# Optimization experiments

Hardware: AMD Instinct MI355X
Metric: run time of the kernel (lower is better)

Reference implementation:

```python
import jax, jax.numpy as jnp
import numpy as np

HEADS = 4
DIM_HEAD = 32
SCALE = DIM_HEAD ** -0.5
EPS = 1e-5


def setup_inputs() -> dict:
    key = jax.random.key(0)
    k1, k2, k3, k4 = jax.random.split(key, 4)
    dim = 256
    hidden = HEADS * DIM_HEAD  # 128
    x = jax.random.normal(k1, (16, dim, 64, 64), dtype=jnp.float32)
    # 1x1 conv weights stored as [out_ch, in_ch] (kernel size 1 squeezed)
    w_qkv = jax.random.normal(k2, (hidden * 3, dim), dtype=jnp.float32) * (dim ** -0.5)
    w_out = jax.random.normal(k3, (dim, hidden), dtype=jnp.float32) * (hidden ** -0.5)
    b_out = jax.random.normal(k4, (dim,), dtype=jnp.float32) * 0.01
    g = jnp.ones((1, dim, 1, 1), dtype=jnp.float32)  # LayerNorm gain
    return {"x": x, "w_qkv": w_qkv, "w_out": w_out, "b_out": b_out, "g": g}


def reference(x, w_qkv, w_out, b_out, g):
    b, c, h, w = x.shape
    n = h * w
    # 1x1 conv to qkv: [b, 3*hidden, h, w]
    qkv = jnp.einsum('oc,bchw->bohw', w_qkv, x)
    q, k, v = jnp.split(qkv, 3, axis=1)

    def to_heads(t):
        return t.reshape(b, HEADS, DIM_HEAD, n)  # b h d n

    q, k, v = to_heads(q), to_heads(k), to_heads(v)
    q = jax.nn.softmax(q, axis=2) * SCALE       # softmax over head-dim d
    k = jax.nn.softmax(k, axis=3)               # softmax over spatial n
    v = v / n                                    # v / (h*w)
    context = jnp.einsum('bhdn,bhen->bhde', k, v)
    out = jnp.einsum('bhde,bhdn->bhen', context, q)  # b h e n
    out = out.reshape(b, HEADS * DIM_HEAD, h, w)
    # output 1x1 conv with bias
    out = jnp.einsum('oc,bchw->bohw', w_out, out) + b_out[None, :, None, None]
    # channel LayerNorm (biased variance over dim=1)
    mean = jnp.mean(out, axis=1, keepdims=True)
    var = jnp.var(out, axis=1, keepdims=True)
    return (out - mean) * jax.lax.rsqrt(var + EPS) * g
```

## Files before the change

kernel.cpp:

```cpp
#include <hip/hip_runtime.h>

typedef short short8 __attribute__((ext_vector_type(8)));
typedef float f32x16 __attribute__((ext_vector_type(16)));
typedef unsigned short ushort_t;

#define B_    16
#define C_    256
#define N_    4096
#define H_    4
#define HID_  128
#define SCALE_ 0.17677669529663687f
#define EPS_  1e-5f

__device__ inline unsigned cvtpk(float a, float b) {
  unsigned r;
  asm("v_cvt_pk_bf16_f32 %0, %1, %2" : "=v"(r) : "v"(a), "v"(b));
  return r;
}

__device__ inline int2 pack4(float a, float b, float c, float d) {
  int2 o;
  o.x = (int)cvtpk(a, b);
  o.y = (int)cvtpk(c, d);
  return o;
}

__device__ inline short8 ld_frag16(const ushort_t* p) {
  return __builtin_bit_cast(short8, *(const int4*)p);
}
__device__ inline short8 ld_frag8(const ushort_t* p) {
  int2 a = *(const int2*)p, b = *(const int2*)(p + 4);
  int4 t; t.x = a.x; t.y = a.y; t.z = b.x; t.w = b.y;
  return __builtin_bit_cast(short8, t);
}

__global__ void k0_wswz(const float* __restrict__ w, ushort_t* __restrict__ wsw) {
  int gid = blockIdx.x * 256 + threadIdx.x;
  int ln = gid & 63, kc = (gid >> 6) & 15, mt = gid >> 10;
  int row = mt * 32 + (ln & 31);
  int col = kc * 16 + (ln >> 5) * 8;
  const float* src = w + (size_t)row * 256 + col;
  float4 a = *(const float4*)src, b = *(const float4*)(src + 4);
  int4 o;
  o.x = (int)cvtpk(a.x, a.y); o.y = (int)cvtpk(a.z, a.w);
  o.z = (int)cvtpk(b.x, b.y); o.w = (int)cvtpk(b.z, b.w);
  *(int4*)(wsw + (size_t)gid * 8) = o;
}

__global__ __launch_bounds__(256, 3) void k1_qkv(
    const float* __restrict__ x, const ushort_t* __restrict__ wsw,
    ushort_t* __restrict__ qp, float* __restrict__ pctx, float* __restrict__ psum)
{
  __shared__ __align__(16) union {
    ushort_t Xs[64 * 264];
    struct { ushort_t kt[128 * 68]; ushort_t vt[128 * 68]; } s2;
  } sm;

  const int tid = threadIdx.x;
  const int b = blockIdx.y;
  const int blk = blockIdx.x;
  const int n0 = blk * 64;
  const int hw = tid >> 6, lane = tid & 63;
  const int half = lane >> 5, lm = lane & 31;

  {
    const float* xsrc = x + (size_t)b * C_ * N_ + n0;
    const int n4 = tid & 15;
    const int cq0 = tid >> 4;
    #pragma unroll
    for (int cc = 0; cc < 4; ++cc) {
      const int cq = cq0 + cc * 16;
      const float* p = xsrc + (size_t)(cq * 4) * N_ + n4 * 4;
      float4 a0 = *(const float4*)(p);
      float4 a1 = *(const float4*)(p + N_);
      float4 a2 = *(const float4*)(p + 2 * N_);
      float4 a3 = *(const float4*)(p + 3 * N_);
      ushort_t* d = sm.Xs + (((cq >> 1) ^ n4) * 8 + (cq & 1) * 4) + (n4 * 4) * 264;
      *(int2*)(d + 0 * 264) = pack4(a0.x, a1.x, a2.x, a3.x);
      *(int2*)(d + 1 * 264) = pack4(a0.y, a1.y, a2.y, a3.y);
      *(int2*)(d + 2 * 264) = pack4(a0.z, a1.z, a2.z, a3.z);
      *(int2*)(d + 3 * 264) = pack4(a0.w, a1.w, a2.w, a3.w);
    }
  }
  __syncthreads();

  f32x16 acc0a, acc0b, acc1a, acc1b, acc2a, acc2b;
  for (int r = 0; r < 16; ++r) {
    acc0a[r] = 0.0f; acc0b[r] = 0.0f; acc1a[r] = 0.0f;
    acc1b[r] = 0.0f; acc2a[r] = 0.0f; acc2b[r] = 0.0f;
  }
  {
    const ushort_t* xrow0 = sm.Xs + lm * 264;
    const ushort_t* xrow1 = sm.Xs + (32 + lm) * 264;
    const int sn0 = lm >> 2;
    const int sn1 = 8 + (lm >> 2);
    const ushort_t* wl = wsw + (size_t)(hw * 16 * 64 + lane) * 8;
    #pragma unroll
    for (int kc = 0; kc < 16; ++kc) {
      short8 b0 = ld_frag16(xrow0 + (((2 * kc + half) ^ sn0) << 3));
      short8 b1 = ld_frag16(xrow1 + (((2 * kc + half) ^ sn1) << 3));
      short8 af0 = ld_frag16(wl + kc * 512);
      short8 af1 = ld_frag16(wl + 32768 + kc * 512);
      short8 af2 = ld_frag16(wl + 65536 + kc * 512);
      acc0a = __builtin_amdgcn_mfma_f32_32x32x16_bf16(af0, b0, acc0a, 0, 0, 0);
      acc0b = __builtin_amdgcn_mfma_f32_32x32x16_bf16(af0, b1, acc0b, 0, 0, 0);
      acc1a = __builtin_amdgcn_mfma_f32_32x32x16_bf16(af1, b0, acc1a, 0, 0, 0);
      acc1b = __builtin_amdgcn_mfma_f32_32x32x16_bf16(af1, b1, acc1b, 0, 0, 0);
      acc2a = __builtin_amdgcn_mfma_f32_32x32x16_bf16(af2, b0, acc2a, 0, 0, 0);
      acc2b = __builtin_amdgcn_mfma_f32_32x32x16_bf16(af2, b1, acc2b, 0, 0, 0);
    }
  }

  __syncthreads();

  for (int r = 0; r < 16; ++r) {
    int row = (r & 3) + 8 * (r >> 2) + 4 * half;
    ushort_t* krow = sm.s2.kt + (hw * 32 + row) * 68;
    ushort_t* vrow = sm.s2.vt + (hw * 32 + row) * 68;
    unsigned kk = cvtpk(__expf(acc1a[r]), __expf(acc1b[r]));
    unsigned vv = cvtpk(acc2a[r], acc2b[r]);
    krow[lm]      = (ushort_t)kk;
    krow[32 + lm] = (ushort_t)(kk >> 16);
    vrow[lm]      = (ushort_t)vv;
    vrow[32 + lm] = (ushort_t)(vv >> 16);
  }
  __syncthreads();

  {
    f32x16 cacc, sacc;
    for (int r = 0; r < 16; ++r) { cacc[r] = 0.0f; sacc[r] = 0.0f; }
    short8 ones;
    #pragma unroll
    for (int j = 0; j < 8; ++j) ones[j] = (short)0x3F80;
    const ushort_t* ka = sm.s2.kt + (hw * 32 + lm) * 68 + half * 8;
    const ushort_t* va = sm.s2.vt + (hw * 32 + lm) * 68 + half * 8;
    #pragma unroll
    for (int ks = 0; ks < 4; ++ks) {
      short8 af = ld_frag8(ka + ks * 16);
      short8 bf = ld_frag8(va + ks * 16);
      cacc = __builtin_amdgcn_mfma_f32_32x32x16_bf16(af, bf, cacc, 0, 0, 0);
      sacc = __builtin_amdgcn_mfma_f32_32x32x16_bf16(af, ones, sacc, 0, 0, 0);
    }

    {
      ushort_t* qpb = qp + (size_t)b * N_ * 128;
      {
        float m = -1e30f;
        for (int r = 0; r < 16; ++r) m = fmaxf(m, acc0a[r]);
        m = fmaxf(m, __shfl_xor(m, 32));
        float qe[16]; float s = 0.0f;
        for (int r = 0; r < 16; ++r) { qe[r] = __expf(acc0a[r] - m); s += qe[r]; }
        s += __shfl_xor(s, 32);
        float sc = SCALE_ / s;
        const int gnt = blk * 2;
        for (int q = 0; q < 4; ++q) {
          int kc = hw * 2 + (q >> 1);
          int fl = (q & 1) * 32 + lm;
          int2 o = pack4(qe[q * 4 + 0] * sc, qe[q * 4 + 1] * sc,
                         qe[q * 4 + 2] * sc, qe[q * 4 + 3] * sc);
          *(int2*)(qpb + (size_t)((gnt * 8 + kc) * 64 + fl) * 8 + 4 * half) = o;
        }
      }
      {
        float m = -1e30f;
        for (int r = 0; r < 16; ++r) m = fmaxf(m, acc0b[r]);
        m = fmaxf(m, __shfl_xor(m, 32));
        float qe[16]; float s = 0.0f;
        for (int r = 0; r < 16; ++r) { qe[r] = __expf(acc0b[r] - m); s += qe[r]; }
        s += __shfl_xor(s, 32);
        float sc = SCALE_ / s;
        const int gnt = blk * 2 + 1;
        for (int q = 0; q < 4; ++q) {
          int kc = hw * 2 + (q >> 1);
          int fl = (q & 1) * 32 + lm;
          int2 o = pack4(qe[q * 4 + 0] * sc, qe[q * 4 + 1] * sc,
                         qe[q * 4 + 2] * sc, qe[q * 4 + 3] * sc);
          *(int2*)(qpb + (size_t)((gnt * 8 + kc) * 64 + fl) * 8 + 4 * half) = o;
        }
      }
    }

    float* pc = pctx + ((size_t)(b * 4 + hw) * 64 + blk) * 1024;
    for (int r = 0; r < 16; ++r) {
      int row = (r & 3) + 8 * (r >> 2) + 4 * half;
      pc[row * 32 + lm] = cacc[r];
    }
    if (lm == 0) {
      float* ps = psum + ((size_t)(b * 4 + hw) * 64 + blk) * 32;
      for (int r = 0; r < 16; ++r) {
        int row = (r & 3) + 8 * (r >> 2) + 4 * half;
        ps[row] = sacc[r];
      }
    }
  }
}

__global__ __launch_bounds__(256) void krw(
    const float* __restrict__ pctx, const float* __restrict__ psum,
    const float* __restrict__ wout, ushort_t* __restrict__ weff)
{
  __shared__ float ctxs[32][32];
  __shared__ float inv[32];
  __shared__ float red[8][32];
  const int tid = threadIdx.x;
  const int bh = blockIdx.x;
  const int pb = bh >> 2, ph = bh & 3;

  {
    const int d = tid & 31, part = tid >> 5;
    const float* ps = psum + (size_t)bh * 2048 + part * 8 * 32 + d;
    float t = 0.0f;
    #pragma unroll
    for (int g = 0; g < 8; ++g) t += ps[g * 32];
    red[part][d] = t;
  }
  float4 s4 = make_float4(0.f, 0.f, 0.f, 0.f);
  {
    const float* pc = pctx + (size_t)bh * 65536 + tid * 4;
    #pragma unroll 8
    for (int c = 0; c < 64; ++c) {
      float4 v = *(const float4*)(pc + c * 1024);
      s4.x += v.x; s4.y += v.y; s4.z += v.z; s4.w += v.w;
    }
  }
  __syncthreads();
  if (tid < 32) {
    float u = 0.0f;
    #pragma unroll
    for (int p = 0; p < 8; ++p) u += red[p][tid];
    inv[tid] = 1.0f / (u * 4096.0f);
  }
  __syncthreads();
  {
    float iv = inv[tid >> 3];
    float* crow = &ctxs[0][0] + tid * 4;
    crow[0] = s4.x * iv; crow[1] = s4.y * iv; crow[2] = s4.z * iv; crow[3] = s4.w * iv;
  }
  __syncthreads();
  {
    const int oc = tid;
    const int mt = oc >> 5, lmm = oc & 31;
    const float* wrow = wout + (size_t)oc * HID_ + ph * 32;
    float wr[32];
    for (int e = 0; e < 32; ++e) wr[e] = wrow[e];
    float vals[32];
    for (int d = 0; d < 32; ++d) {
      float s = 0.0f;
      for (int e = 0; e < 32; ++e) s += wr[e] * ctxs[d][e];
      vals[d] = s;
    }
    ushort_t* wb_b = weff + (size_t)pb * 32768;
    for (int kci = 0; kci < 2; ++kci) {
      int kc = ph * 2 + kci;
      for (int hf = 0; hf < 2; ++hf) {
        int d0 = kci * 16 + hf * 8;
        int4 o;
        o.x = (int)cvtpk(vals[d0 + 0], vals[d0 + 1]);
        o.y = (int)cvtpk(vals[d0 + 2], vals[d0 + 3]);
        o.z = (int)cvtpk(vals[d0 + 4], vals[d0 + 5]);
        o.w = (int)cvtpk(vals[d0 + 6], vals[d0 + 7]);
        *(int4*)(wb_b + (size_t)((mt * 8 + kc) * 64 + hf * 32 + lmm) * 8) = o;
      }
    }
  }
}

__global__ __launch_bounds__(256, 4) void k3_out(
    const ushort_t* __restrict__ weff, const ushort_t* __restrict__ qp,
    const float* __restrict__ bout, const float* __restrict__ g,
    float* __restrict__ out)
{
  __shared__ float part_s[2][64], part_s2[2][64];
  __shared__ float st_mu[64], st_rs[64];

  const int tid = threadIdx.x;
  const int b = blockIdx.y;
  const int blk = blockIdx.x;
  const int n0 = blk * 64;
  const int w = tid >> 6, lane = tid & 63;
  const int half = lane >> 5, lm = lane & 31;
  const int ntile = w & 1, mgrp = w >> 1;
  const int gnt = blk * 2 + ntile;

  f32x16 acc[4];
  for (int i = 0; i < 4; ++i)
    for (int r = 0; r < 16; ++r) acc[i][r] = 0.0f;

  {
    const ushort_t* qb = qp + (size_t)b * N_ * 128 + (size_t)gnt * 8 * 64 * 8;
    const ushort_t* wbase = weff + (size_t)b * 32768 + ((size_t)(mgrp * 4) * 8 * 64 + lane) * 8;
    for (int kc = 0; kc < 8; ++kc) {
      short8 bfrag = ld_frag16(qb + (size_t)(kc * 64 + lane) * 8);
      for (int i = 0; i < 4; ++i) {
        short8 af = ld_frag16(wbase + (size_t)((i * 8 + kc) * 64) * 8);
        acc[i] = __builtin_amdgcn_mfma_f32_32x32x16_bf16(af, bfrag, acc[i], 0, 0, 0);
      }
    }
  }

  float s = 0.0f, s2v = 0.0f;
  for (int i = 0; i < 4; ++i) {
    int mt = mgrp * 4 + i;
    for (int r = 0; r < 16; ++r) {
      int row = mt * 32 + (r & 3) + 8 * (r >> 2) + 4 * half;
      acc[i][r] += bout[row];
      float v = acc[i][r];
      s += v; s2v += v * v;
    }
  }
  s += __shfl_xor(s, 32);
  s2v += __shfl_xor(s2v, 32);
  if (half == 0) { part_s[mgrp][ntile * 32 + lm] = s; part_s2[mgrp][ntile * 32 + lm] = s2v; }
  __syncthreads();
  if (tid < 64) {
    float S = part_s[0][tid] + part_s[1][tid];
    float S2 = part_s2[0][tid] + part_s2[1][tid];
    float mu = S * (1.0f / 256.0f);
    float var = S2 * (1.0f / 256.0f) - mu * mu;
    st_mu[tid] = mu;
    st_rs[tid] = rsqrtf(var + EPS_);
  }
  __syncthreads();

  const int col = ntile * 32 + lm;
  const float mu = st_mu[col];
  const float rs = st_rs[col];
  float* ob = out + (size_t)b * C_ * N_ + n0 + col;
  for (int i = 0; i < 4; ++i) {
    int mt = mgrp * 4 + i;
    for (int r = 0; r < 16; ++r) {
      int row = mt * 32 + (r & 3) + 8 * (r >> 2) + 4 * half;
      ob[(size_t)row * N_] = (acc[i][r] - mu) * rs * g[row];
    }
  }
}

extern "C" void kernel_launch(void* const* d_in, const int* in_sizes, int n_in,
                              void* d_out, int out_size, void* d_ws, size_t ws_size,
                              hipStream_t stream) {
  (void)in_sizes; (void)n_in; (void)out_size; (void)ws_size;
  const float* x    = (const float*)d_in[0];
  const float* wqkv = (const float*)d_in[1];
  const float* wout = (const float*)d_in[2];
  const float* bout = (const float*)d_in[3];
  const float* g    = (const float*)d_in[4];
  float* out = (float*)d_out;

  char* ws = (char*)d_ws;
  ushort_t* qp    = (ushort_t*)(ws);
  float*    pctx  = (float*)(ws + ((size_t)16 << 20));
  float*    psum  = (float*)(ws + ((size_t)32 << 20));
  ushort_t* weff  = (ushort_t*)(ws + ((size_t)32 << 20) + (512 << 10));
  ushort_t* wsw   = (ushort_t*)(ws + ((size_t)33 << 20) + (512 << 10));

  k0_wswz<<<48, 256, 0, stream>>>(wqkv, wsw);
  k1_qkv<<<dim3(64, 16), 256, 0, stream>>>(x, wsw, qp, pctx, psum);
  krw<<<64, 256, 0, stream>>>(pctx, psum, wout, weff);
  k3_out<<<dim3(64, 16), 256, 0, stream>>>(weff, qp, bout, g, out);
}
```

Baseline: 175.9 us.

## Split context reduction into wider kernel and move q softmax before LDS sync

The old krw kernel reduced 64 partial context tiles per batch-head using only 64 blocks. That work is now done by a separate reduce kernel with 256 blocks, and a small second kernel builds the effective output weights. The q softmax and store in k1 are moved ahead of the barrier so their global writes overlap the k/v LDS staging and context MFMAs. The cost is an extra kernel launch and an extra workspace round trip for the reduced context.

```diff
diff --git a/kernel.cpp b/kernel.cpp
--- a/kernel.cpp
+++ b/kernel.cpp
@@ -111,6 +111,44 @@
     }
   }
 
+  {
+    ushort_t* qpb = qp + (size_t)b * N_ * 128;
+    {
+      float m = -1e30f;
+      for (int r = 0; r < 16; ++r) m = fmaxf(m, acc0a[r]);
+      m = fmaxf(m, __shfl_xor(m, 32));
+      float qe[16]; float s = 0.0f;
+      for (int r = 0; r < 16; ++r) { qe[r] = __expf(acc0a[r] - m); s += qe[r]; }
+      s += __shfl_xor(s, 32);
+      float sc = SCALE_ / s;
+      const int gnt = blk * 2;
+      for (int q = 0; q < 4; ++q) {
+        int kc = hw * 2 + (q >> 1);
+        int fl = (q & 1) * 32 + lm;
+        int2 o = pack4(qe[q * 4 + 0] * sc, qe[q * 4 + 1] * sc,
+                       qe[q * 4 + 2] * sc, qe[q * 4 + 3] * sc);
+        *(int2*)(qpb + (size_t)((gnt * 8 + kc) * 64 + fl) * 8 + 4 * half) = o;
+      }
+    }
+    {
+      float m = -1e30f;
+      for (int r = 0; r < 16; ++r) m = fmaxf(m, acc0b[r]);
+      m = fmaxf(m, __shfl_xor(m, 32));
+      float qe[16]; float s = 0.0f;
+      for (int r = 0; r < 16; ++r) { qe[r] = __expf(acc0b[r] - m); s += qe[r]; }
+      s += __shfl_xor(s, 32);
+      float sc = SCALE_ / s;
+      const int gnt = blk * 2 + 1;
+      for (int q = 0; q < 4; ++q) {
+        int kc = hw * 2 + (q >> 1);
+        int fl = (q & 1) * 32 + lm;
+        int2 o = pack4(qe[q * 4 + 0] * sc, qe[q * 4 + 1] * sc,
+                       qe[q * 4 + 2] * sc, qe[q * 4 + 3] * sc);
+        *(int2*)(qpb + (size_t)((gnt * 8 + kc) * 64 + fl) * 8 + 4 * half) = o;
+      }
+    }
+  }
+
   __syncthreads();
 
   for (int r = 0; r < 16; ++r) {
@@ -141,45 +179,6 @@
       cacc = __builtin_amdgcn_mfma_f32_32x32x16_bf16(af, bf, cacc, 0, 0, 0);
       sacc = __builtin_amdgcn_mfma_f32_32x32x16_bf16(af, ones, sacc, 0, 0, 0);
     }
-
-    {
-      ushort_t* qpb = qp + (size_t)b * N_ * 128;
-      {
-        float m = -1e30f;
-        for (int r = 0; r < 16; ++r) m = fmaxf(m, acc0a[r]);
-        m = fmaxf(m, __shfl_xor(m, 32));
-        float qe[16]; float s = 0.0f;
-        for (int r = 0; r < 16; ++r) { qe[r] = __expf(acc0a[r] - m); s += qe[r]; }
-        s += __shfl_xor(s, 32);
-        float sc = SCALE_ / s;
-        const int gnt = blk * 2;
-        for (int q = 0; q < 4; ++q) {
-          int kc = hw * 2 + (q >> 1);
-          int fl = (q & 1) * 32 + lm;
-          int2 o = pack4(qe[q * 4 + 0] * sc, qe[q * 4 + 1] * sc,
-                         qe[q * 4 + 2] * sc, qe[q * 4 + 3] * sc);
-          *(int2*)(qpb + (size_t)((gnt * 8 + kc) * 64 + fl) * 8 + 4 * half) = o;
-        }
-      }
-      {
-        float m = -1e30f;
-        for (int r = 0; r < 16; ++r) m = fmaxf(m, acc0b[r]);
-        m = fmaxf(m, __shfl_xor(m, 32));
-        float qe[16]; float s = 0.0f;
-        for (int r = 0; r < 16; ++r) { qe[r] = __expf(acc0b[r] - m); s += qe[r]; }
-        s += __shfl_xor(s, 32);
-        float sc = SCALE_ / s;
-        const int gnt = blk * 2 + 1;
-        for (int q = 0; q < 4; ++q) {
-          int kc = hw * 2 + (q >> 1);
-          int fl = (q & 1) * 32 + lm;
-          int2 o = pack4(qe[q * 4 + 0] * sc, qe[q * 4 + 1] * sc,
-                         qe[q * 4 + 2] * sc, qe[q * 4 + 3] * sc);
-          *(int2*)(qpb + (size_t)((gnt * 8 + kc) * 64 + fl) * 8 + 4 * half) = o;
-        }
-      }
-    }
-
     float* pc = pctx + ((size_t)(b * 4 + hw) * 64 + blk) * 1024;
     for (int r = 0; r < 16; ++r) {
       int row = (r & 3) + 8 * (r >> 2) + 4 * half;
@@ -195,46 +194,53 @@
   }
 }
 
-__global__ __launch_bounds__(256) void krw(
+__global__ __launch_bounds__(256) void kr_reduce(
     const float* __restrict__ pctx, const float* __restrict__ psum,
+    float* __restrict__ ctxr, float* __restrict__ psumr)
+{
+  __shared__ float red[8][32];
+  const int tid = threadIdx.x;
+  const int q = blockIdx.x;
+  const int bh = blockIdx.y;
+  const int idx = q * 256 + tid;
+  const float* src = pctx + (size_t)bh * 65536 + idx;
+  float s = 0.0f;
+  #pragma unroll 8
+  for (int blk = 0; blk < 64; ++blk) s += src[blk * 1024];
+  ctxr[(size_t)bh * 1024 + idx] = s;
+  if (q == 0) {
+    const int d = tid & 31, part = tid >> 5;
+    const float* ps = psum + (size_t)bh * 2048 + part * 8 * 32 + d;
+    float t = 0.0f;
+    #pragma unroll
+    for (int g = 0; g < 8; ++g) t += ps[g * 32];
+    red[part][d] = t;
+    __syncthreads();
+    if (tid < 32) {
+      float u = 0.0f;
+      #pragma unroll
+      for (int p = 0; p < 8; ++p) u += red[p][tid];
+      psumr[(size_t)bh * 32 + tid] = u;
+    }
+  }
+}
+
+__global__ __launch_bounds__(256) void k2b_weff(
+    const float* __restrict__ ctxr, const float* __restrict__ psumr,
     const float* __restrict__ wout, ushort_t* __restrict__ weff)
 {
   __shared__ float ctxs[32][32];
   __shared__ float inv[32];
-  __shared__ float red[8][32];
   const int tid = threadIdx.x;
-  const int bh = blockIdx.x;
-  const int pb = bh >> 2, ph = bh & 3;
-
-  {
-    const int d = tid & 31, part = tid >> 5;
-    const float* ps = psum + (size_t)bh * 2048 + part * 8 * 32 + d;
-    float t = 0.0f;
-    #pragma unroll
-    for (int g = 0; g < 8; ++g) t += ps[g * 32];
-    red[part][d] = t;
-  }
-  float4 s4 = make_float4(0.f, 0.f, 0.f, 0.f);
-  {
-    const float* pc = pctx + (size_t)bh * 65536 + tid * 4;
-    #pragma unroll 8
-    for (int c = 0; c < 64; ++c) {
-      float4 v = *(const float4*)(pc + c * 1024);
-      s4.x += v.x; s4.y += v.y; s4.z += v.z; s4.w += v.w;
-    }
-  }
-  __syncthreads();
-  if (tid < 32) {
-    float u = 0.0f;
-    #pragma unroll
-    for (int p = 0; p < 8; ++p) u += red[p][tid];
-    inv[tid] = 1.0f / (u * 4096.0f);
-  }
+  const int ph = blockIdx.x, pb = blockIdx.y;
+  const size_t bh = (size_t)(pb * 4 + ph);
+  float4 v = *(const float4*)(ctxr + bh * 1024 + tid * 4);
+  if (tid < 32) inv[tid] = 1.0f / (psumr[bh * 32 + tid] * 4096.0f);
   __syncthreads();
   {
     float iv = inv[tid >> 3];
     float* crow = &ctxs[0][0] + tid * 4;
-    crow[0] = s4.x * iv; crow[1] = s4.y * iv; crow[2] = s4.z * iv; crow[3] = s4.w * iv;
+    crow[0] = v.x * iv; crow[1] = v.y * iv; crow[2] = v.z * iv; crow[3] = v.w * iv;
   }
   __syncthreads();
   {
@@ -352,9 +358,12 @@
   float*    psum  = (float*)(ws + ((size_t)32 << 20));
   ushort_t* weff  = (ushort_t*)(ws + ((size_t)32 << 20) + (512 << 10));
   ushort_t* wsw   = (ushort_t*)(ws + ((size_t)33 << 20) + (512 << 10));
+  float*    ctxr  = (float*)(ws + ((size_t)34 << 20));
+  float*    psumr = (float*)(ws + ((size_t)34 << 20) + (256 << 10));
 
   k0_wswz<<<48, 256, 0, stream>>>(wqkv, wsw);
   k1_qkv<<<dim3(64, 16), 256, 0, stream>>>(x, wsw, qp, pctx, psum);
-  krw<<<64, 256, 0, stream>>>(pctx, psum, wout, weff);
+  kr_reduce<<<dim3(4, 64), 256, 0, stream>>>(pctx, psum, ctxr, psumr);
+  k2b_weff<<<dim3(4, 16), 256, 0, stream>>>(ctxr, psumr, wout, weff);
   k3_out<<<dim3(64, 16), 256, 0, stream>>>(weff, qp, bout, g, out);
 }
```

New measurement: 158.5 us. -9.9%, faster.
